# Performance work log

Measured on AMD Instinct MI355X. Metric: run time of the kernel, lower is better.

## Reference

```python
import jax, jax.numpy as jnp
import numpy as np

B, M, D = 8, 2048, 1024


def setup_inputs() -> dict:
    key = jax.random.key(0)
    kx, kq, kk, kv = jax.random.split(key, 4)
    x = jax.random.normal(kx, (B, M, D), dtype=jnp.float32)
    wq = jax.random.normal(kq, (D, D), dtype=jnp.float32) * 0.02
    wk = jax.random.normal(kk, (D, D), dtype=jnp.float32) * 0.02
    wv = jax.random.normal(kv, (D, D), dtype=jnp.float32) * 0.02
    return {"x": x, "wq": wq, "wk": wk, "wv": wv}


def _rope_tables(m, d):
    # theta_i = 10000^(-2*(i-1)/d)  (faithful to original, including the (i-1))
    i = jnp.arange(d // 2, dtype=jnp.float32)
    theta = jnp.power(jnp.float32(10000.0), -2.0 * (i - 1.0) / d)
    ang = jnp.arange(m, dtype=jnp.float32)[:, None] * theta[None, :]  # [m, d/2]
    return jnp.cos(ang), jnp.sin(ang)


def _rotate(t, cos, sin):
    # t: [b, m, d]. Equivalent to t[pos] @ R[pos] with R the block-diag 2x2 rotations:
    # out[2i]   =  t[2i]*cos_i + t[2i+1]*sin_i
    # out[2i+1] = -t[2i]*sin_i + t[2i+1]*cos_i
    te, to = t[..., 0::2], t[..., 1::2]
    re = te * cos + to * sin
    ro = -te * sin + to * cos
    return jnp.stack([re, ro], axis=-1).reshape(t.shape)


def reference(x, wq, wk, wv):
    b, m, d = x.shape
    q = x @ wq.T  # nn.Linear: y = x W^T
    k = x @ wk.T
    v = x @ wv.T
    cos, sin = _rope_tables(m, d)
    qr = _rotate(q, cos, sin)
    kr = _rotate(k, cos, sin)
    scale = 1.0 / jnp.sqrt(jnp.float32(d))
    scores = jnp.einsum('bqd,bkd->bqk', qr, kr) * scale  # [b, m, m]
    attn = jax.nn.softmax(scores, axis=-1)
    return jnp.einsum('bqk,bkd->bqd', attn, v)
```

## Files before the change

### kernel.cpp

```cpp
#include <hip/hip_runtime.h>
#include <hip/hip_bf16.h>
#include <cstdint>
#include <type_traits>

typedef unsigned short u16;
typedef __attribute__((ext_vector_type(8))) short short8;
typedef __attribute__((ext_vector_type(4))) float floatx4;

__device__ __forceinline__ u16 f2bf(float f) {
  union { float f; uint32_t u; } v; v.f = f;
  uint32_t u = v.u;
  return (u16)((u + 0x7FFFu + ((u >> 16) & 1u)) >> 16);
}
__device__ __forceinline__ float bf2f(u16 h) {
  union { uint32_t u; float f; } v; v.u = ((uint32_t)h) << 16;
  return v.f;
}

typedef const __attribute__((address_space(1))) char GChar;
typedef __attribute__((address_space(3))) char LChar;
__device__ __forceinline__ void gload_lds16(const void* g, void* l) {
  __builtin_amdgcn_global_load_lds((GChar*)g, (LChar*)l, 16, 0, 0);
}

__global__ void cast_f32_bf16(const float* __restrict__ src, u16* __restrict__ dst, int n) {
  int i = (blockIdx.x * blockDim.x + threadIdx.x) * 4;
  int stride = gridDim.x * blockDim.x * 4;
  for (; i < n; i += stride) {
    float4 v = *reinterpret_cast<const float4*>(src + i);
    ushort4 o;
    o.x = f2bf(v.x); o.y = f2bf(v.y); o.z = f2bf(v.z); o.w = f2bf(v.w);
    *reinterpret_cast<ushort4*>(dst + i) = o;
  }
}

__global__ void rope_tables(float* __restrict__ cosT, float* __restrict__ sinT) {
  int idx = blockIdx.x * blockDim.x + threadIdx.x;
  int m = idx >> 9;
  int i = idx & 511;
  double ex = -2.0 * ((double)i - 1.0) / 1024.0;
  double theta = exp(ex * log(10000.0));
  double ang = (double)m * theta;
  cosT[idx] = (float)cos(ang);
  sinT[idx] = (float)sin(ang);
}

template <typename CT>
__global__ __launch_bounds__(256) void gemm_bt(
    const u16* __restrict__ A, const u16* __restrict__ Bw, CT* __restrict__ C,
    int K, long lda, long ldb, long ldc,
    long strideA, long strideB, long strideC, float scale)
{
  __shared__ u16 As[128 * 32];
  __shared__ u16 Bs[128 * 32];

  const int bz = blockIdx.z;
  A  += (long)bz * strideA;
  Bw += (long)bz * strideB;
  C  += (long)bz * strideC;

  const int tm = blockIdx.y, tn = blockIdx.x;
  const int t = threadIdx.x;
  const int lane = t & 63, wave = t >> 6;
  const int wm = (wave >> 1) * 64, wn = (wave & 1) * 64;

  const int srow = t >> 2;
  const int scol = (t & 3) * 8;
  const u16* Ag = A + (long)(tm * 128 + srow) * lda + scol;
  const u16* Bg = Bw + (long)(tn * 128 + srow) * ldb + scol;
  u16* AsW = As + wave * 512;
  u16* BsW = Bs + wave * 512;

  floatx4 acc[4][4];
#pragma unroll
  for (int m = 0; m < 4; ++m)
#pragma unroll
    for (int n = 0; n < 4; ++n) acc[m][n] = (floatx4){0.f, 0.f, 0.f, 0.f};

  const int arow = (lane & 15) * 32 + ((lane >> 4) * 8);
  const int nk = K >> 5;
  for (int kt = 0; kt < nk; ++kt) {
    __syncthreads();
    const u16* ag = Ag + kt * 32;
    const u16* bg = Bg + kt * 32;
    gload_lds16(ag,             AsW);
    gload_lds16(ag + 64 * lda,  AsW + 2048);
    gload_lds16(bg,             BsW);
    gload_lds16(bg + 64 * ldb,  BsW + 2048);
    __syncthreads();

    short8 af[4], bf[4];
#pragma unroll
    for (int m = 0; m < 4; ++m)
      af[m] = *reinterpret_cast<const short8*>(&As[(wm + m * 16) * 32 + arow]);
#pragma unroll
    for (int n = 0; n < 4; ++n)
      bf[n] = *reinterpret_cast<const short8*>(&Bs[(wn + n * 16) * 32 + arow]);
#pragma unroll
    for (int m = 0; m < 4; ++m)
#pragma unroll
      for (int n = 0; n < 4; ++n)
        acc[m][n] = __builtin_amdgcn_mfma_f32_16x16x32_bf16(af[m], bf[n], acc[m][n], 0, 0, 0);
  }

  const long crow = (long)tm * 128 + wm + ((lane >> 4) << 2);
  const long ccol = (long)tn * 128 + wn + (lane & 15);
#pragma unroll
  for (int m = 0; m < 4; ++m)
#pragma unroll
    for (int n = 0; n < 4; ++n)
#pragma unroll
      for (int r = 0; r < 4; ++r) {
        long row = crow + m * 16 + r;
        long col = ccol + n * 16;
        float val = acc[m][n][r] * scale;
        if constexpr (std::is_same<CT, u16>::value)
          C[row * ldc + col] = f2bf(val);
        else
          C[row * ldc + col] = val;
      }
}

__global__ void rope_apply(u16* __restrict__ qkv,
                           const float* __restrict__ cosT, const float* __restrict__ sinT) {
  int g = blockIdx.x * blockDim.x + threadIdx.x;
  int row = g >> 7;
  int grp = g & 127;
  int m = row & 2047;
  int p0 = grp * 4;
  float4 c = *reinterpret_cast<const float4*>(&cosT[m * 512 + p0]);
  float4 s = *reinterpret_cast<const float4*>(&sinT[m * 512 + p0]);
  float cc[4] = {c.x, c.y, c.z, c.w};
  float ss[4] = {s.x, s.y, s.z, s.w};
  long base = (long)row * 3072 + p0 * 2;
#pragma unroll
  for (int h = 0; h < 2; ++h) {
    u16* p = qkv + base + h * 1024;
    short8 v = *reinterpret_cast<const short8*>(p);
    short8 o;
#pragma unroll
    for (int j = 0; j < 4; ++j) {
      float te = bf2f((u16)v[2 * j]);
      float to = bf2f((u16)v[2 * j + 1]);
      float re = te * cc[j] + to * ss[j];
      float ro = -te * ss[j] + to * cc[j];
      o[2 * j] = (short)f2bf(re);
      o[2 * j + 1] = (short)f2bf(ro);
    }
    *reinterpret_cast<short8*>(p) = o;
  }
}

__global__ void transpose_v(const u16* __restrict__ qkv, u16* __restrict__ vt) {
  __shared__ u16 tile[32][33];
  int b = blockIdx.z;
  int m0 = blockIdx.y * 32, d0 = blockIdx.x * 32;
  int tx = threadIdx.x & 31, ty = threadIdx.x >> 5;
#pragma unroll
  for (int r = ty; r < 32; r += 8)
    tile[r][tx] = qkv[(long)(b * 2048 + m0 + r) * 3072 + 2048 + d0 + tx];
  __syncthreads();
#pragma unroll
  for (int r = ty; r < 32; r += 8)
    vt[(long)b * 1024 * 2048 + (long)(d0 + r) * 2048 + m0 + tx] = tile[tx][r];
}

__global__ __launch_bounds__(256) void softmax_rows_bf16(u16* __restrict__ S) {
  const long base = (long)blockIdx.x * 2048;
  const int t = threadIdx.x, lane = t & 63, wave = t >> 6;
  short8 in8 = *reinterpret_cast<const short8*>(&S[base + t * 8]);
  float v[8];
#pragma unroll
  for (int j = 0; j < 8; ++j) v[j] = bf2f((u16)in8[j]);
  float mx = v[0];
#pragma unroll
  for (int j = 1; j < 8; ++j) mx = fmaxf(mx, v[j]);
#pragma unroll
  for (int o = 32; o; o >>= 1) mx = fmaxf(mx, __shfl_xor(mx, o, 64));
  __shared__ float redm[4], reds[4];
  if (lane == 0) redm[wave] = mx;
  __syncthreads();
  mx = fmaxf(fmaxf(redm[0], redm[1]), fmaxf(redm[2], redm[3]));
  float sm = 0.f;
#pragma unroll
  for (int j = 0; j < 8; ++j) { v[j] = __expf(v[j] - mx); sm += v[j]; }
#pragma unroll
  for (int o = 32; o; o >>= 1) sm += __shfl_xor(sm, o, 64);
  if (lane == 0) reds[wave] = sm;
  __syncthreads();
  float inv = 1.0f / (reds[0] + reds[1] + reds[2] + reds[3]);
  short8 o8;
#pragma unroll
  for (int j = 0; j < 8; ++j) o8[j] = (short)f2bf(v[j] * inv);
  *reinterpret_cast<short8*>(&S[base + t * 8]) = o8;
}

extern "C" void kernel_launch(void* const* d_in, const int* in_sizes, int n_in,
                              void* d_out, int out_size, void* d_ws, size_t ws_size,
                              hipStream_t stream) {
  const float* x  = (const float*)d_in[0];
  const float* wq = (const float*)d_in[1];
  const float* wk = (const float*)d_in[2];
  const float* wv = (const float*)d_in[3];
  float* out = (float*)d_out;
  char* ws = (char*)d_ws;

  u16*  xb   = (u16*)(ws);
  u16*  vt   = (u16*)(ws);
  u16*  wcat = (u16*)(ws + 33554432);
  float* cosT = (float*)(ws + 39845888);
  float* sinT = (float*)(ws + 44040192);
  u16*  qkv  = (u16*)(ws + 48234496);
  u16*  S    = (u16*)(ws + 148897792);
  const size_t NEED = 216006656;
  if (ws_size < NEED) return;

  cast_f32_bf16<<<2048, 256, 0, stream>>>(x, xb, 16384 * 1024);
  cast_f32_bf16<<<256, 256, 0, stream>>>(wq, wcat, 1024 * 1024);
  cast_f32_bf16<<<256, 256, 0, stream>>>(wk, wcat + 1024 * 1024, 1024 * 1024);
  cast_f32_bf16<<<256, 256, 0, stream>>>(wv, wcat + 2 * 1024 * 1024, 1024 * 1024);
  rope_tables<<<(2048 * 512) / 256, 256, 0, stream>>>(cosT, sinT);

  gemm_bt<u16><<<dim3(24, 128, 1), 256, 0, stream>>>(
      xb, wcat, qkv, 1024, 1024, 1024, 3072, 0, 0, 0, 1.0f);

  rope_apply<<<(16384 * 128) / 256, 256, 0, stream>>>(qkv, cosT, sinT);
  transpose_v<<<dim3(32, 64, 8), 256, 0, stream>>>(qkv, vt);

  gemm_bt<u16><<<dim3(16, 16, 8), 256, 0, stream>>>(
      qkv, qkv + 1024, S, 1024, 3072, 3072, 2048,
      2048L * 3072, 2048L * 3072, 2048L * 2048, 0.03125f);

  softmax_rows_bf16<<<16384, 256, 0, stream>>>(S);

  gemm_bt<float><<<dim3(8, 16, 8), 256, 0, stream>>>(
      S, vt, out, 2048, 2048, 2048, 1024,
      2048L * 2048, 1024L * 2048, 2048L * 1024, 1.0f);
}
```

Baseline: 547.7 us.

## Fuse RoPE into QKV GEMM epilogue and add XCD-aware block swizzle

```diff
diff --git a/kernel.cpp b/kernel.cpp
--- a/kernel.cpp
+++ b/kernel.cpp
@@ -21,6 +21,11 @@
 typedef __attribute__((address_space(3))) char LChar;
 __device__ __forceinline__ void gload_lds16(const void* g, void* l) {
   __builtin_amdgcn_global_load_lds((GChar*)g, (LChar*)l, 16, 0, 0);
+}
+
+__device__ __forceinline__ int xcd_swz(int id, int nwg) {
+  int cpx = nwg >> 3;
+  return (id & 7) * cpx + (id >> 3);
 }
 
 __global__ void cast_f32_bf16(const float* __restrict__ src, u16* __restrict__ dst, int n) {
@@ -49,7 +54,8 @@
 __global__ __launch_bounds__(256) void gemm_bt(
     const u16* __restrict__ A, const u16* __restrict__ Bw, CT* __restrict__ C,
     int K, long lda, long ldb, long ldc,
-    long strideA, long strideB, long strideC, float scale)
+    long strideA, long strideB, long strideC, float scale,
+    const float* __restrict__ cosT, const float* __restrict__ sinT, int ropeCols)
 {
   __shared__ u16 As[128 * 32];
   __shared__ u16 Bs[128 * 32];
@@ -59,7 +65,10 @@
   Bw += (long)bz * strideB;
   C  += (long)bz * strideC;
 
-  const int tm = blockIdx.y, tn = blockIdx.x;
+  const int nwg = gridDim.x * gridDim.y;
+  const int swz = xcd_swz(blockIdx.y * gridDim.x + blockIdx.x, nwg);
+  const int tm = swz % gridDim.y, tn = swz / gridDim.y;
+
   const int t = threadIdx.x;
   const int lane = t & 63, wave = t >> 6;
   const int wm = (wave >> 1) * 64, wn = (wave & 1) * 64;
@@ -105,6 +114,8 @@
 
   const long crow = (long)tm * 128 + wm + ((lane >> 4) << 2);
   const long ccol = (long)tn * 128 + wn + (lane & 15);
+  const bool doRope = (ropeCols > 0) && (tn * 128 < ropeCols);
+  const int par = lane & 1;
 #pragma unroll
   for (int m = 0; m < 4; ++m)
 #pragma unroll
@@ -114,41 +125,19 @@
         long row = crow + m * 16 + r;
         long col = ccol + n * 16;
         float val = acc[m][n][r] * scale;
+        if (doRope) {
+          float other = __shfl_xor(val, 1, 64);
+          int i  = ((int)(col & 1023)) >> 1;
+          int mm = (int)(row & 2047);
+          float c = cosT[mm * 512 + i];
+          float s = sinT[mm * 512 + i];
+          val = par ? (val * c - other * s) : (val * c + other * s);
+        }
         if constexpr (std::is_same<CT, u16>::value)
           C[row * ldc + col] = f2bf(val);
         else
           C[row * ldc + col] = val;
       }
-}
-
-__global__ void rope_apply(u16* __restrict__ qkv,
-                           const float* __restrict__ cosT, const float* __restrict__ sinT) {
-  int g = blockIdx.x * blockDim.x + threadIdx.x;
-  int row = g >> 7;
-  int grp = g & 127;
-  int m = row & 2047;
-  int p0 = grp * 4;
-  float4 c = *reinterpret_cast<const float4*>(&cosT[m * 512 + p0]);
-  float4 s = *reinterpret_cast<const float4*>(&sinT[m * 512 + p0]);
-  float cc[4] = {c.x, c.y, c.z, c.w};
-  float ss[4] = {s.x, s.y, s.z, s.w};
-  long base = (long)row * 3072 + p0 * 2;
-#pragma unroll
-  for (int h = 0; h < 2; ++h) {
-    u16* p = qkv + base + h * 1024;
-    short8 v = *reinterpret_cast<const short8*>(p);
-    short8 o;
-#pragma unroll
-    for (int j = 0; j < 4; ++j) {
-      float te = bf2f((u16)v[2 * j]);
-      float to = bf2f((u16)v[2 * j + 1]);
-      float re = te * cc[j] + to * ss[j];
-      float ro = -te * ss[j] + to * cc[j];
-      o[2 * j] = (short)f2bf(re);
-      o[2 * j + 1] = (short)f2bf(ro);
-    }
-    *reinterpret_cast<short8*>(p) = o;
-  }
 }
 
 __global__ void transpose_v(const u16* __restrict__ qkv, u16* __restrict__ vt) {
@@ -222,18 +211,20 @@
   rope_tables<<<(2048 * 512) / 256, 256, 0, stream>>>(cosT, sinT);
 
   gemm_bt<u16><<<dim3(24, 128, 1), 256, 0, stream>>>(
-      xb, wcat, qkv, 1024, 1024, 1024, 3072, 0, 0, 0, 1.0f);
-
-  rope_apply<<<(16384 * 128) / 256, 256, 0, stream>>>(qkv, cosT, sinT);
+      xb, wcat, qkv, 1024, 1024, 1024, 3072, 0, 0, 0, 1.0f,
+      cosT, sinT, 2048);
+
   transpose_v<<<dim3(32, 64, 8), 256, 0, stream>>>(qkv, vt);
 
   gemm_bt<u16><<<dim3(16, 16, 8), 256, 0, stream>>>(
       qkv, qkv + 1024, S, 1024, 3072, 3072, 2048,
-      2048L * 3072, 2048L * 3072, 2048L * 2048, 0.03125f);
+      2048L * 3072, 2048L * 3072, 2048L * 2048, 0.03125f,
+      nullptr, nullptr, 0);
 
   softmax_rows_bf16<<<16384, 256, 0, stream>>>(S);
 
   gemm_bt<float><<<dim3(8, 16, 8), 256, 0, stream>>>(
       S, vt, out, 2048, 2048, 2048, 1024,
-      2048L * 2048, 1024L * 2048, 2048L * 1024, 1.0f);
-}
+      2048L * 2048, 1024L * 2048, 2048L * 1024, 1.0f,
+      nullptr, nullptr, 0);
+}
```

Result: slower. 590.4 us (+7.8%).

## Replace 128x128 GEMM with double-buffered swizzled 256x256 tile kernel

Applied to the files above, without the earlier changes.

```diff
diff --git a/kernel.cpp b/kernel.cpp
--- a/kernel.cpp
+++ b/kernel.cpp
@@ -43,82 +43,6 @@
   double ang = (double)m * theta;
   cosT[idx] = (float)cos(ang);
   sinT[idx] = (float)sin(ang);
-}
-
-template <typename CT>
-__global__ __launch_bounds__(256) void gemm_bt(
-    const u16* __restrict__ A, const u16* __restrict__ Bw, CT* __restrict__ C,
-    int K, long lda, long ldb, long ldc,
-    long strideA, long strideB, long strideC, float scale)
-{
-  __shared__ u16 As[128 * 32];
-  __shared__ u16 Bs[128 * 32];
-
-  const int bz = blockIdx.z;
-  A  += (long)bz * strideA;
-  Bw += (long)bz * strideB;
-  C  += (long)bz * strideC;
-
-  const int tm = blockIdx.y, tn = blockIdx.x;
-  const int t = threadIdx.x;
-  const int lane = t & 63, wave = t >> 6;
-  const int wm = (wave >> 1) * 64, wn = (wave & 1) * 64;
-
-  const int srow = t >> 2;
-  const int scol = (t & 3) * 8;
-  const u16* Ag = A + (long)(tm * 128 + srow) * lda + scol;
-  const u16* Bg = Bw + (long)(tn * 128 + srow) * ldb + scol;
-  u16* AsW = As + wave * 512;
-  u16* BsW = Bs + wave * 512;
-
-  floatx4 acc[4][4];
-#pragma unroll
-  for (int m = 0; m < 4; ++m)
-#pragma unroll
-    for (int n = 0; n < 4; ++n) acc[m][n] = (floatx4){0.f, 0.f, 0.f, 0.f};
-
-  const int arow = (lane & 15) * 32 + ((lane >> 4) * 8);
-  const int nk = K >> 5;
-  for (int kt = 0; kt < nk; ++kt) {
-    __syncthreads();
-    const u16* ag = Ag + kt * 32;
-    const u16* bg = Bg + kt * 32;
-    gload_lds16(ag,             AsW);
-    gload_lds16(ag + 64 * lda,  AsW + 2048);
-    gload_lds16(bg,             BsW);
-    gload_lds16(bg + 64 * ldb,  BsW + 2048);
-    __syncthreads();
-
-    short8 af[4], bf[4];
-#pragma unroll
-    for (int m = 0; m < 4; ++m)
-      af[m] = *reinterpret_cast<const short8*>(&As[(wm + m * 16) * 32 + arow]);
-#pragma unroll
-    for (int n = 0; n < 4; ++n)
-      bf[n] = *reinterpret_cast<const short8*>(&Bs[(wn + n * 16) * 32 + arow]);
-#pragma unroll
-    for (int m = 0; m < 4; ++m)
-#pragma unroll
-      for (int n = 0; n < 4; ++n)
-        acc[m][n] = __builtin_amdgcn_mfma_f32_16x16x32_bf16(af[m], bf[n], acc[m][n], 0, 0, 0);
-  }
-
-  const long crow = (long)tm * 128 + wm + ((lane >> 4) << 2);
-  const long ccol = (long)tn * 128 + wn + (lane & 15);
-#pragma unroll
-  for (int m = 0; m < 4; ++m)
-#pragma unroll
-    for (int n = 0; n < 4; ++n)
-#pragma unroll
-      for (int r = 0; r < 4; ++r) {
-        long row = crow + m * 16 + r;
-        long col = ccol + n * 16;
-        float val = acc[m][n][r] * scale;
-        if constexpr (std::is_same<CT, u16>::value)
-          C[row * ldc + col] = f2bf(val);
-        else
-          C[row * ldc + col] = val;
-      }
 }
 
 __global__ void rope_apply(u16* __restrict__ qkv,
@@ -142,13 +66,144 @@
     for (int j = 0; j < 4; ++j) {
       float te = bf2f((u16)v[2 * j]);
       float to = bf2f((u16)v[2 * j + 1]);
-      float re = te * cc[j] + to * ss[j];
-      float ro = -te * ss[j] + to * cc[j];
-      o[2 * j] = (short)f2bf(re);
-      o[2 * j + 1] = (short)f2bf(ro);
+      o[2 * j]     = (short)f2bf(te * cc[j] + to * ss[j]);
+      o[2 * j + 1] = (short)f2bf(-te * ss[j] + to * cc[j]);
     }
     *reinterpret_cast<short8*>(p) = o;
   }
+}
+
+template <typename CT>
+__global__ __launch_bounds__(512, 2) void gemm256(
+    const u16* __restrict__ A, const u16* __restrict__ Bw, CT* __restrict__ C,
+    int K, long lda, long ldb, long ldc,
+    long strideA, long strideB, long strideC, float scale)
+{
+  __shared__ u16 lds[65536];
+
+  const int bz = blockIdx.z;
+  A  += (long)bz * strideA;
+  Bw += (long)bz * strideB;
+  C  += (long)bz * strideC;
+
+  const int tm = blockIdx.y, tn = blockIdx.x;
+  const int t = threadIdx.x;
+  const int lane = t & 63, wave = t >> 6;
+  const int wm = wave >> 2, wn = wave & 3;
+
+  const long arow0 = (long)tm * 256;
+  const long brow0 = (long)tn * 256;
+
+  const int sr  = t >> 3;
+  const int scs = ((t & 7) * 8) ^ (((sr >> 2) & 3) << 4);
+
+  u16* const Ab0 = lds;
+  u16* const Ab1 = lds + 16384;
+  u16* const Bb0 = lds + 32768;
+  u16* const Bb1 = lds + 49152;
+
+  const int Xr = (((lane & 15) >> 2) & 3) << 4;
+  const int kc = (lane >> 4) * 8;
+
+  floatx4 acc[8][4];
+#pragma unroll
+  for (int m = 0; m < 8; ++m)
+#pragma unroll
+    for (int n = 0; n < 4; ++n) acc[m][n] = (floatx4){0.f, 0.f, 0.f, 0.f};
+
+  const int nkt = K >> 6;
+
+#pragma unroll
+  for (int h = 0; h < 2; ++h) {
+    const u16* g = Bw + (brow0 + h * 128 + sr) * ldb + scs;
+    u16* d = Bb0 + h * 8192 + t * 8;
+    gload_lds16(g, d);
+    gload_lds16(g + 64 * ldb, d + 4096);
+  }
+#pragma unroll
+  for (int h = 0; h < 2; ++h) {
+    const u16* g = A + (arow0 + h * 128 + sr) * lda + scs;
+    u16* d = Ab0 + h * 8192 + t * 8;
+    gload_lds16(g, d);
+    gload_lds16(g + 64 * lda, d + 4096);
+  }
+
+  for (int kt = 0; kt < nkt; ++kt) {
+    u16* const Ac = (kt & 1) ? Ab1 : Ab0;
+    u16* const Bc = (kt & 1) ? Bb1 : Bb0;
+    u16* const An = (kt & 1) ? Ab0 : Ab1;
+    u16* const Bn = (kt & 1) ? Bb0 : Bb1;
+    const bool pf = (kt + 1 < nkt);
+    const int kn = (kt + 1) * 64;
+
+    short8 bfr[4][2];
+
+#pragma unroll
+    for (int q = 0; q < 4; ++q) {
+      if (pf) {
+        if (q < 2) {
+          const u16* g = Bw + (brow0 + q * 128 + sr) * ldb + kn + scs;
+          u16* d = Bn + q * 8192 + t * 8;
+          gload_lds16(g, d);
+          gload_lds16(g + 64 * ldb, d + 4096);
+        } else {
+          const int h = q - 2;
+          const u16* g = A + (arow0 + h * 128 + sr) * lda + kn + scs;
+          u16* d = An + h * 8192 + t * 8;
+          gload_lds16(g, d);
+          gload_lds16(g + 64 * lda, d + 4096);
+        }
+      }
+      if (q == 0) {
+        if (pf) asm volatile("s_waitcnt vmcnt(2)" ::: "memory");
+        else    asm volatile("s_waitcnt vmcnt(0)" ::: "memory");
+        __builtin_amdgcn_s_barrier();
+#pragma unroll
+        for (int n = 0; n < 4; ++n)
+#pragma unroll
+          for (int kk = 0; kk < 2; ++kk)
+            bfr[n][kk] = *reinterpret_cast<const short8*>(
+                &Bc[(wn * 64 + n * 16 + (lane & 15)) * 64 + ((kk * 32 + kc) ^ Xr)]);
+      }
+      short8 afr[2][2];
+#pragma unroll
+      for (int i = 0; i < 2; ++i)
+#pragma unroll
+        for (int kk = 0; kk < 2; ++kk)
+          afr[i][kk] = *reinterpret_cast<const short8*>(
+              &Ac[(wm * 128 + (2 * q + i) * 16 + (lane & 15)) * 64 + ((kk * 32 + kc) ^ Xr)]);
+
+      __builtin_amdgcn_s_barrier();
+      __builtin_amdgcn_s_setprio(1);
+#pragma unroll
+      for (int i = 0; i < 2; ++i)
+#pragma unroll
+        for (int kk = 0; kk < 2; ++kk)
+#pragma unroll
+          for (int n = 0; n < 4; ++n)
+            acc[2 * q + i][n] = __builtin_amdgcn_mfma_f32_16x16x32_bf16(
+                afr[i][kk], bfr[n][kk], acc[2 * q + i][n], 0, 0, 0);
+      __builtin_amdgcn_s_setprio(0);
+      __builtin_amdgcn_s_barrier();
+    }
+  }
+
+  const long crow = arow0 + wm * 128 + ((lane >> 4) << 2);
+  const long ccol = brow0 + wn * 64 + (lane & 15);
+#pragma unroll
+  for (int m = 0; m < 8; ++m)
+#pragma unroll
+    for (int n = 0; n < 4; ++n)
+#pragma unroll
+      for (int r = 0; r < 4; ++r) {
+        float val = acc[m][n][r] * scale;
+        long row = crow + m * 16 + r;
+        long col = ccol + n * 16;
+        if constexpr (std::is_same<CT, u16>::value)
+          C[row * ldc + col] = f2bf(val);
+        else
+          C[row * ldc + col] = val;
+      }
 }
 
 __global__ void transpose_v(const u16* __restrict__ qkv, u16* __restrict__ vt) {
@@ -221,19 +276,19 @@
   cast_f32_bf16<<<256, 256, 0, stream>>>(wv, wcat + 2 * 1024 * 1024, 1024 * 1024);
   rope_tables<<<(2048 * 512) / 256, 256, 0, stream>>>(cosT, sinT);
 
-  gemm_bt<u16><<<dim3(24, 128, 1), 256, 0, stream>>>(
+  gemm256<u16><<<dim3(12, 64, 1), 512, 0, stream>>>(
       xb, wcat, qkv, 1024, 1024, 1024, 3072, 0, 0, 0, 1.0f);
 
   rope_apply<<<(16384 * 128) / 256, 256, 0, stream>>>(qkv, cosT, sinT);
   transpose_v<<<dim3(32, 64, 8), 256, 0, stream>>>(qkv, vt);
 
-  gemm_bt<u16><<<dim3(16, 16, 8), 256, 0, stream>>>(
+  gemm256<u16><<<dim3(8, 8, 8), 512, 0, stream>>>(
       qkv, qkv + 1024, S, 1024, 3072, 3072, 2048,
       2048L * 3072, 2048L * 3072, 2048L * 2048, 0.03125f);
 
   softmax_rows_bf16<<<16384, 256, 0, stream>>>(S);
 
-  gemm_bt<float><<<dim3(8, 16, 8), 256, 0, stream>>>(
+  gemm256<float><<<dim3(4, 8, 8), 512, 0, stream>>>(
       S, vt, out, 2048, 2048, 2048, 1024,
       2048L * 2048, 1024L * 2048, 2048L * 1024, 1.0f);
 }
```

Result: faster. 468.9 us (-14.4%).
